# Performance work log

Measured on AMD Instinct MI355X. Metric: run time of the kernel, lower is better.

## Reference

```python
import jax, jax.numpy as jnp
import numpy as np

EMB = 1024
HEADS = 16
DH = EMB // HEADS


def setup_inputs() -> dict:
    key = jax.random.key(0)
    ks = jax.random.split(key, 9)
    B, S = 4, 2048
    scale = 1.0 / np.sqrt(EMB)
    x = jax.random.normal(ks[0], (B, S, EMB), dtype=jnp.float32)
    Wq = jax.random.normal(ks[1], (EMB, EMB), dtype=jnp.float32) * scale
    Wk = jax.random.normal(ks[2], (EMB, EMB), dtype=jnp.float32) * scale
    Wv = jax.random.normal(ks[3], (EMB, EMB), dtype=jnp.float32) * scale
    Wo = jax.random.normal(ks[4], (EMB, EMB), dtype=jnp.float32) * scale
    bq = jnp.zeros((EMB,), jnp.float32)
    bk = jnp.zeros((EMB,), jnp.float32)
    bv = jnp.zeros((EMB,), jnp.float32)
    bo = jnp.zeros((EMB,), jnp.float32)
    return {"x": x, "Wq": Wq, "bq": bq, "Wk": Wk, "bk": bk,
            "Wv": Wv, "bv": bv, "Wo": Wo, "bo": bo}


def _split_heads(t):
    B, S, _ = t.shape
    return t.reshape(B, S, HEADS, DH).transpose(0, 2, 1, 3)  # [B,H,S,Dh]


def reference(x, Wq, bq, Wk, bk, Wv, bv, Wo, bo):
    q = _split_heads(x @ Wq + bq)
    k = _split_heads(x @ Wk + bk)
    v = _split_heads(x @ Wv + bv)
    # scaled dot-product attention, full [B,H,S,S] score matrix as in source
    logits = jnp.einsum("bhqd,bhkd->bhqk", q, k) / jnp.sqrt(jnp.float32(DH))
    attn = jax.nn.softmax(logits, axis=-1)
    ctx = jnp.einsum("bhqk,bhkd->bhqd", attn, v)
    B, _, S, _ = ctx.shape
    concat = ctx.transpose(0, 2, 1, 3).reshape(B, S, EMB)
    return concat @ Wo + bo
```

## Files before the change

### kernel.cpp

```cpp
#include <hip/hip_runtime.h>
#include <hip/hip_bf16.h>
#include <stdint.h>

typedef __bf16 bf16;
typedef __bf16 bf16x4 __attribute__((ext_vector_type(4)));
typedef __bf16 bf16x8 __attribute__((ext_vector_type(8)));
typedef float f32x4 __attribute__((ext_vector_type(4)));

__device__ __forceinline__ void async_ld16(const void* g, void* l) {
  __builtin_amdgcn_global_load_lds(
      (__attribute__((address_space(1))) void*)(void*)(g),
      (__attribute__((address_space(3))) void*)(l), 16, 0, 0);
}

__device__ __forceinline__ bf16 fast_bf16(float f) {
  uint32_t u = (__float_as_uint(f) + 0x8000u) >> 16;
  union { uint16_t s; bf16 b; } cv;
  cv.s = (uint16_t)u;
  return cv.b;
}

__device__ __forceinline__ uint32_t pack_bf16(float lo, float hi) {
  return __builtin_amdgcn_perm(__float_as_uint(hi) + 0x8000u,
                               __float_as_uint(lo) + 0x8000u, 0x07060302u);
}

__global__ __launch_bounds__(256) void cast_f32_bf16(const float* __restrict__ in,
                                                     bf16* __restrict__ out, int n) {
  int i = (blockIdx.x * 256 + threadIdx.x) * 4;
  if (i < n) {
    float4 f = *(const float4*)(in + i);
    uint2 o;
    o.x = pack_bf16(f.x, f.y);
    o.y = pack_bf16(f.z, f.w);
    *(uint2*)(out + i) = o;
  }
}

__global__ __launch_bounds__(256) void transpose_weights(const float* __restrict__ Wq,
                                                         const float* __restrict__ Wk,
                                                         const float* __restrict__ Wv,
                                                         const float* __restrict__ Wo,
                                                         bf16* __restrict__ Wt,
                                                         bf16* __restrict__ Wot) {
  __shared__ bf16 tile[64][66];
  int z = blockIdx.z;
  const float* src = z == 0 ? Wq : (z == 1 ? Wk : (z == 2 ? Wv : Wo));
  bf16* dst = z == 0 ? Wt : (z == 1 ? Wt + 1048576 : (z == 2 ? Wt + 2097152 : Wot));
  int r0 = blockIdx.x * 64, c0 = blockIdx.y * 64;
  int t = threadIdx.x;
#pragma unroll
  for (int i = 0; i < 16; ++i) {
    int idx = t + i * 256;
    int r = idx >> 6, c = idx & 63;
    tile[r][c] = fast_bf16(src[(size_t)(r0 + r) * 1024 + (c0 + c)]);
  }
  __syncthreads();
#pragma unroll
  for (int i = 0; i < 16; ++i) {
    int idx = t + i * 256;
    int c = idx >> 6, r = idx & 63;
    dst[(size_t)(c0 + c) * 1024 + (r0 + r)] = tile[r][c];
  }
}

__device__ __forceinline__ void gemm128_mainloop(const bf16* __restrict__ A,
                                                 const bf16* __restrict__ Bt, int K,
                                                 int rowBase, int colBase,
                                                 bf16* As, bf16* Bs,
                                                 f32x4 (&acc)[4][4]) {
  int t = threadIdx.x, lane = t & 63, w = t >> 6;
  int wM = w >> 1, wN = w & 1, quad = lane >> 4, l15 = lane & 15;
  int r_off = lane >> 3;
  int c_sw = (((lane & 7) ^ r_off) << 3);
  int sw = l15 & 7;
  for (int k0 = 0; k0 < K; k0 += 64) {
    __syncthreads();
#pragma unroll
    for (int i = 0; i < 4; ++i) {
      int e = i * 2048 + w * 512;
      int row = (e >> 6) + r_off;
      async_ld16(A + (size_t)(rowBase + row) * K + (k0 + c_sw), As + e);
      async_ld16(Bt + (size_t)(colBase + row) * K + (k0 + c_sw), Bs + e);
    }
    __syncthreads();
#pragma unroll
    for (int ks = 0; ks < 2; ++ks) {
      int co = (((ks * 4 + quad) ^ sw) << 3);
      bf16x8 af[4], bfr[4];
#pragma unroll
      for (int mi = 0; mi < 4; ++mi)
        af[mi] = *(const bf16x8*)(As + (wM * 64 + mi * 16 + l15) * 64 + co);
#pragma unroll
      for (int ni = 0; ni < 4; ++ni)
        bfr[ni] = *(const bf16x8*)(Bs + (wN * 64 + ni * 16 + l15) * 64 + co);
#pragma unroll
      for (int mi = 0; mi < 4; ++mi)
#pragma unroll
        for (int ni = 0; ni < 4; ++ni)
          acc[mi][ni] = __builtin_amdgcn_mfma_f32_16x16x32_bf16(af[mi], bfr[ni], acc[mi][ni], 0, 0, 0);
    }
  }
}

__global__ __launch_bounds__(512, 2) void gemm_qkv(const bf16* __restrict__ X,
                                                   const bf16* __restrict__ Wt,
                                                   const float* __restrict__ bq,
                                                   const float* __restrict__ bk,
                                                   const float* __restrict__ bv,
                                                   bf16* __restrict__ Qo,
                                                   bf16* __restrict__ Ko,
                                                   bf16* __restrict__ Vto) {
  __shared__ alignas(16) bf16 smem[2][24576];

  int t = threadIdx.x, lane = t & 63, w = t >> 6;
  int wM = w >> 1, wN = w & 1, quad = lane >> 4, l15 = lane & 15;
  int r_off = lane >> 3;
  int c_sw = (((lane & 7) ^ r_off) << 3);
  int sw = l15 & 7;
  int rowBase = blockIdx.y * 256, colBase = blockIdx.x * 128;

  f32x4 acc[4][4];
  f32x4 z = {0.f, 0.f, 0.f, 0.f};
#pragma unroll
  for (int mi = 0; mi < 4; ++mi)
#pragma unroll
    for (int ni = 0; ni < 4; ++ni) acc[mi][ni] = z;

#pragma unroll
  for (int i = 0; i < 4; ++i) {
    int e = (w * 4 + i) * 512;
    int row = (e >> 6) + r_off;
    async_ld16(X + (size_t)(rowBase + row) * 1024 + c_sw, smem[0] + e);
  }
#pragma unroll
  for (int i = 0; i < 2; ++i) {
    int e = (w * 2 + i) * 512;
    int row = (e >> 6) + r_off;
    async_ld16(Wt + (size_t)(colBase + row) * 1024 + c_sw, smem[0] + 16384 + e);
  }
  __syncthreads();

  for (int kt = 0; kt < 16; ++kt) {
    int cur = kt & 1;
    const bf16* As = smem[cur];
    const bf16* Bs = smem[cur] + 16384;
    bf16* Asn = smem[cur ^ 1];
    bf16* Bsn = smem[cur ^ 1] + 16384;
    int kn = (kt + 1) * 64;

    bf16x8 af[4], bfr[2];

    if (kt < 15) {
#pragma unroll
      for (int i = 0; i < 4; ++i) {
        int e = (w * 4 + i) * 512;
        int row = (e >> 6) + r_off;
        async_ld16(X + (size_t)(rowBase + row) * 1024 + (kn + c_sw), Asn + e);
      }
    }
    {
      int co = ((quad ^ sw) << 3);
#pragma unroll
      for (int mi = 0; mi < 4; ++mi)
        af[mi] = *(const bf16x8*)(As + (wM * 64 + mi * 16 + l15) * 64 + co);
      bfr[0] = *(const bf16x8*)(Bs + (wN * 64 + l15) * 64 + co);
      bfr[1] = *(const bf16x8*)(Bs + (wN * 64 + 16 + l15) * 64 + co);
      asm volatile("s_waitcnt lgkmcnt(0)" ::: "memory");
      __builtin_amdgcn_sched_barrier(0);
      __builtin_amdgcn_s_setprio(1);
#pragma unroll
      for (int mi = 0; mi < 4; ++mi) {
        acc[mi][0] = __builtin_amdgcn_mfma_f32_16x16x32_bf16(af[mi], bfr[0], acc[mi][0], 0, 0, 0);
        acc[mi][1] = __builtin_amdgcn_mfma_f32_16x16x32_bf16(af[mi], bfr[1], acc[mi][1], 0, 0, 0);
      }
      __builtin_amdgcn_s_setprio(0);
    }

    if (kt < 15) {
#pragma unroll
      for (int i = 0; i < 2; ++i) {
        int e = (w * 2 + i) * 512;
        int row = (e >> 6) + r_off;
        async_ld16(Wt + (size_t)(colBase + row) * 1024 + (kn + c_sw), Bsn + e);
      }
    }
    {
      int co = ((quad ^ sw) << 3);
      bfr[0] = *(const bf16x8*)(Bs + (wN * 64 + 32 + l15) * 64 + co);
      bfr[1] = *(const bf16x8*)(Bs + (wN * 64 + 48 + l15) * 64 + co);
      asm volatile("s_waitcnt lgkmcnt(0)" ::: "memory");
      __builtin_amdgcn_sched_barrier(0);
      __builtin_amdgcn_s_setprio(1);
#pragma unroll
      for (int mi = 0; mi < 4; ++mi) {
        acc[mi][2] = __builtin_amdgcn_mfma_f32_16x16x32_bf16(af[mi], bfr[0], acc[mi][2], 0, 0, 0);
        acc[mi][3] = __builtin_amdgcn_mfma_f32_16x16x32_bf16(af[mi], bfr[1], acc[mi][3], 0, 0, 0);
      }
      __builtin_amdgcn_s_setprio(0);
    }

    {
      int co = (((4 + quad) ^ sw) << 3);
#pragma unroll
      for (int mi = 0; mi < 4; ++mi)
        af[mi] = *(const bf16x8*)(As + (wM * 64 + mi * 16 + l15) * 64 + co);
      bfr[0] = *(const bf16x8*)(Bs + (wN * 64 + l15) * 64 + co);
      bfr[1] = *(const bf16x8*)(Bs + (wN * 64 + 16 + l15) * 64 + co);
      asm volatile("s_waitcnt lgkmcnt(0)" ::: "memory");
      __builtin_amdgcn_sched_barrier(0);
      __builtin_amdgcn_s_setprio(1);
#pragma unroll
      for (int mi = 0; mi < 4; ++mi) {
        acc[mi][0] = __builtin_amdgcn_mfma_f32_16x16x32_bf16(af[mi], bfr[0], acc[mi][0], 0, 0, 0);
        acc[mi][1] = __builtin_amdgcn_mfma_f32_16x16x32_bf16(af[mi], bfr[1], acc[mi][1], 0, 0, 0);
      }
      __builtin_amdgcn_s_setprio(0);
    }

    {
      int co = (((4 + quad) ^ sw) << 3);
      bfr[0] = *(const bf16x8*)(Bs + (wN * 64 + 32 + l15) * 64 + co);
      bfr[1] = *(const bf16x8*)(Bs + (wN * 64 + 48 + l15) * 64 + co);
      asm volatile("s_waitcnt lgkmcnt(0)" ::: "memory");
      __builtin_amdgcn_sched_barrier(0);
      __builtin_amdgcn_s_setprio(1);
#pragma unroll
      for (int mi = 0; mi < 4; ++mi) {
        acc[mi][2] = __builtin_amdgcn_mfma_f32_16x16x32_bf16(af[mi], bfr[0], acc[mi][2], 0, 0, 0);
        acc[mi][3] = __builtin_amdgcn_mfma_f32_16x16x32_bf16(af[mi], bfr[1], acc[mi][3], 0, 0, 0);
      }
      __builtin_amdgcn_s_setprio(0);
    }

    __syncthreads();
  }

  int which = colBase >> 10;
  int baseh = (colBase & 1023) >> 6;
  int b = rowBase >> 11, s0 = rowBase & 2047;
  bf16* ep = smem[0];

  if (which == 2) {
#pragma unroll
    for (int hp = 0; hp < 2; ++hp) {
      __syncthreads();
      if (wN == hp) {
#pragma unroll
        for (int mi = 0; mi < 4; ++mi)
#pragma unroll
          for (int ni = 0; ni < 4; ++ni) {
            int d = ni * 16 + l15;
            float bb = bv[(colBase & 1023) + hp * 64 + d];
            int sl = wM * 64 + mi * 16 + quad * 4;
            uint2 pv;
            pv.x = pack_bf16(acc[mi][ni][0] + bb, acc[mi][ni][1] + bb);
            pv.y = pack_bf16(acc[mi][ni][2] + bb, acc[mi][ni][3] + bb);
            *(uint2*)(ep + d * 264 + sl) = pv;
          }
      }
      __syncthreads();
      int hg = baseh + hp;
#pragma unroll
      for (int it = 0; it < 4; ++it) {
        int idx = t + it * 512;
        int d = idx >> 5, c = idx & 31;
        bf16x8 vv = *(const bf16x8*)(ep + d * 264 + c * 8);
        *(bf16x8*)(Vto + (((size_t)((b << 4) + hg) << 6) + d) * 2048 + s0 + c * 8) = vv;
      }
    }
  } else {
    const float* bias = which == 0 ? bq : bk;
    bf16* dst = which == 0 ? Qo : Ko;
    float scale = which == 0 ? 0.125f * 1.44269504f : 1.0f;
#pragma unroll
    for (int hp = 0; hp < 2; ++hp) {
      __syncthreads();
      if (wN == hp) {
#pragma unroll
        for (int mi = 0; mi < 4; ++mi)
#pragma unroll
          for (int ni = 0; ni < 4; ++ni) {
            int d = ni * 16 + l15;
            float bb = bias[(colBase & 1023) + hp * 64 + d];
            int m = wM * 64 + mi * 16 + quad * 4;
#pragma unroll
            for (int r = 0; r < 4; ++r)
              ep[(m + r) * 72 + d] = fast_bf16((acc[mi][ni][r] + bb) * scale);
          }
      }
      __syncthreads();
      int hg = baseh + hp;
      bf16* gbase = dst + ((((size_t)((b << 4) + hg)) * 2048 + s0) << 6);
#pragma unroll
      for (int it = 0; it < 4; ++it) {
        int idx = t + it * 512;
        int m = idx >> 3, c = idx & 7;
        bf16x8 vv = *(const bf16x8*)(ep + m * 72 + c * 8);
        *(bf16x8*)(gbase + m * 64 + c * 8) = vv;
      }
    }
  }
}

__global__ __launch_bounds__(256) void gemm_out(const bf16* __restrict__ Cb,
                                                const bf16* __restrict__ Wot,
                                                const float* __restrict__ bo,
                                                float* __restrict__ out) {
  __shared__ alignas(16) bf16 As[128 * 64];
  __shared__ alignas(16) bf16 Bs[128 * 64];
  f32x4 acc[4][4];
  f32x4 z = {0.f, 0.f, 0.f, 0.f};
#pragma unroll
  for (int mi = 0; mi < 4; ++mi)
#pragma unroll
    for (int ni = 0; ni < 4; ++ni) acc[mi][ni] = z;
  int rowBase = blockIdx.y * 128, colBase = blockIdx.x * 128;
  gemm128_mainloop(Cb, Wot, 1024, rowBase, colBase, As, Bs, acc);

  int t = threadIdx.x, lane = t & 63, w = t >> 6;
  int wM = w >> 1, wN = w & 1, quad = lane >> 4, l15 = lane & 15;
#pragma unroll
  for (int mi = 0; mi < 4; ++mi)
#pragma unroll
    for (int ni = 0; ni < 4; ++ni) {
      int n = colBase + wN * 64 + ni * 16 + l15;
      float bb = bo[n];
#pragma unroll
      for (int r = 0; r < 4; ++r) {
        int m = rowBase + wM * 64 + mi * 16 + quad * 4 + r;
        out[(size_t)m * 1024 + n] = acc[mi][ni][r] + bb;
      }
    }
}

__global__ __launch_bounds__(256, 2) void attn(const bf16* __restrict__ Q,
                                               const bf16* __restrict__ Kg,
                                               const bf16* __restrict__ Vt,
                                               bf16* __restrict__ ctx) {
  __shared__ alignas(16) bf16 QPs[256 * 64];
  __shared__ alignas(16) bf16 Ks[2][4096];
  __shared__ alignas(16) bf16 Vs[2][4096];

  int t = threadIdx.x, lane = t & 63, w = t >> 6;
  int quad = lane >> 4, l15 = lane & 15;
  int r_off = lane >> 3;
  int c_sw = (((lane & 7) ^ r_off) << 3);
  int sw = l15 & 7;
  int bh = blockIdx.x;
  int q0 = blockIdx.y * 256;
  const bf16* Qp = Q + ((size_t)bh * 2048 + q0) * 64;
  const bf16* Kp = Kg + (size_t)bh * 2048 * 64;
  const bf16* Vp = Vt + (size_t)bh * 64 * 2048;

#pragma unroll
  for (int i = 0; i < 8; ++i) {
    int e = w * 4096 + i * 512;
    int row = (e >> 6) + r_off;
    async_ld16(Qp + (size_t)row * 64 + c_sw, QPs + e);
  }
#pragma unroll
  for (int i = 0; i < 2; ++i) {
    int e = w * 1024 + i * 512;
    int row = (e >> 6) + r_off;
    async_ld16(Kp + (size_t)row * 64 + c_sw, Ks[0] + e);
    async_ld16(Vp + (size_t)row * 2048 + c_sw, Vs[0] + e);
  }
  __syncthreads();

  bf16x8 qf[2][4];
#pragma unroll
  for (int ks = 0; ks < 2; ++ks)
#pragma unroll
    for (int qi = 0; qi < 4; ++qi)
      qf[ks][qi] = *(const bf16x8*)(QPs + (w * 64 + qi * 16 + l15) * 64 + (((ks * 4 + quad) ^ sw) << 3));
  asm volatile("s_waitcnt lgkmcnt(0)" ::: "memory");

  bf16* Ps = QPs + w * 4096;

  bf16 one1 = (bf16)1.0f;
  bf16x8 ones = {one1, one1, one1, one1, one1, one1, one1, one1};

  f32x4 o[4][4];
  f32x4 ol[4];
  f32x4 z = {0.f, 0.f, 0.f, 0.f};
#pragma unroll
  for (int mi = 0; mi < 4; ++mi) {
    ol[mi] = z;
#pragma unroll
    for (int ni = 0; ni < 4; ++ni) o[mi][ni] = z;
  }

  for (int kt = 0; kt < 32; ++kt) {
    int cur = kt & 1;
    if (kt < 31) {
      int kn = (kt + 1) * 64;
#pragma unroll
      for (int i = 0; i < 2; ++i) {
        int e = w * 1024 + i * 512;
        int row = (e >> 6) + r_off;
        async_ld16(Kp + (size_t)(kn + row) * 64 + c_sw, Ks[cur ^ 1] + e);
        async_ld16(Vp + (size_t)row * 2048 + kn + c_sw, Vs[cur ^ 1] + e);
      }
    }
    const bf16* Kc = Ks[cur];
    const bf16* Vc = Vs[cur];

    f32x4 sA[2][4];
#pragma unroll
    for (int ki = 0; ki < 2; ++ki)
#pragma unroll
      for (int qi = 0; qi < 4; ++qi) sA[ki][qi] = z;
    __builtin_amdgcn_s_setprio(1);
#pragma unroll
    for (int ks = 0; ks < 2; ++ks) {
      int co = (((ks * 4 + quad) ^ sw) << 3);
      bf16x8 kf0 = *(const bf16x8*)(Kc + (l15) * 64 + co);
      bf16x8 kf1 = *(const bf16x8*)(Kc + (16 + l15) * 64 + co);
#pragma unroll
      for (int qi = 0; qi < 4; ++qi) {
        sA[0][qi] = __builtin_amdgcn_mfma_f32_16x16x32_bf16(kf0, qf[ks][qi], sA[0][qi], 0, 0, 0);
        sA[1][qi] = __builtin_amdgcn_mfma_f32_16x16x32_bf16(kf1, qf[ks][qi], sA[1][qi], 0, 0, 0);
      }
    }
    __builtin_amdgcn_s_setprio(0);
#pragma unroll
    for (int qi = 0; qi < 4; ++qi)
#pragma unroll
      for (int ki = 0; ki < 2; ++ki) {
        float p0 = __builtin_amdgcn_exp2f(sA[ki][qi][0]);
        float p1 = __builtin_amdgcn_exp2f(sA[ki][qi][1]);
        float p2 = __builtin_amdgcn_exp2f(sA[ki][qi][2]);
        float p3 = __builtin_amdgcn_exp2f(sA[ki][qi][3]);
        uint2 pb;
        pb.x = pack_bf16(p0, p1);
        pb.y = pack_bf16(p2, p3);
        int cs = (ki * 2 + (quad >> 1)) ^ sw;
        *(uint2*)(Ps + (qi * 16 + l15) * 64 + cs * 8 + (quad & 1) * 4) = pb;
      }

    f32x4 sB[2][4];
#pragma unroll
    for (int ki = 0; ki < 2; ++ki)
#pragma unroll
      for (int qi = 0; qi < 4; ++qi) sB[ki][qi] = z;
    __builtin_amdgcn_s_setprio(1);
#pragma unroll
    for (int ks = 0; ks < 2; ++ks) {
      int co = (((ks * 4 + quad) ^ sw) << 3);
      bf16x8 kf2 = *(const bf16x8*)(Kc + (32 + l15) * 64 + co);
      bf16x8 kf3 = *(const bf16x8*)(Kc + (48 + l15) * 64 + co);
#pragma unroll
      for (int qi = 0; qi < 4; ++qi) {
        sB[0][qi] = __builtin_amdgcn_mfma_f32_16x16x32_bf16(kf2, qf[ks][qi], sB[0][qi], 0, 0, 0);
        sB[1][qi] = __builtin_amdgcn_mfma_f32_16x16x32_bf16(kf3, qf[ks][qi], sB[1][qi], 0, 0, 0);
      }
    }
    __builtin_amdgcn_s_setprio(0);

    asm volatile("s_waitcnt lgkmcnt(0)" ::: "memory");

    {
      int co = ((quad ^ sw) << 3);
      bf16x8 pf[4], vf[4];
#pragma unroll
      for (int mi = 0; mi < 4; ++mi)
        pf[mi] = *(const bf16x8*)(Ps + (mi * 16 + l15) * 64 + co);
#pragma unroll
      for (int ni = 0; ni < 4; ++ni)
        vf[ni] = *(const bf16x8*)(Vc + (ni * 16 + l15) * 64 + co);
      __builtin_amdgcn_s_setprio(1);
#pragma unroll
      for (int mi = 0; mi < 4; ++mi) {
#pragma unroll
        for (int ni = 0; ni < 4; ++ni)
          o[mi][ni] = __builtin_amdgcn_mfma_f32_16x16x32_bf16(pf[mi], vf[ni], o[mi][ni], 0, 0, 0);
        ol[mi] = __builtin_amdgcn_mfma_f32_16x16x32_bf16(pf[mi], ones, ol[mi], 0, 0, 0);
      }
      __builtin_amdgcn_s_setprio(0);
    }

#pragma unroll
    for (int qi = 0; qi < 4; ++qi)
#pragma unroll
      for (int ki = 0; ki < 2; ++ki) {
        float p0 = __builtin_amdgcn_exp2f(sB[ki][qi][0]);
        float p1 = __builtin_amdgcn_exp2f(sB[ki][qi][1]);
        float p2 = __builtin_amdgcn_exp2f(sB[ki][qi][2]);
        float p3 = __builtin_amdgcn_exp2f(sB[ki][qi][3]);
        uint2 pb;
        pb.x = pack_bf16(p0, p1);
        pb.y = pack_bf16(p2, p3);
        int cs = (ki * 2 + 4 + (quad >> 1)) ^ sw;
        *(uint2*)(Ps + (qi * 16 + l15) * 64 + cs * 8 + (quad & 1) * 4) = pb;
      }

    asm volatile("s_waitcnt lgkmcnt(0)" ::: "memory");

    {
      int co = (((4 + quad) ^ sw) << 3);
      bf16x8 pf[4], vf[4];
#pragma unroll
      for (int mi = 0; mi < 4; ++mi)
        pf[mi] = *(const bf16x8*)(Ps + (mi * 16 + l15) * 64 + co);
#pragma unroll
      for (int ni = 0; ni < 4; ++ni)
        vf[ni] = *(const bf16x8*)(Vc + (ni * 16 + l15) * 64 + co);
      __builtin_amdgcn_s_setprio(1);
#pragma unroll
      for (int mi = 0; mi < 4; ++mi) {
#pragma unroll
        for (int ni = 0; ni < 4; ++ni)
          o[mi][ni] = __builtin_amdgcn_mfma_f32_16x16x32_bf16(pf[mi], vf[ni], o[mi][ni], 0, 0, 0);
        ol[mi] = __builtin_amdgcn_mfma_f32_16x16x32_bf16(pf[mi], ones, ol[mi], 0, 0, 0);
      }
      __builtin_amdgcn_s_setprio(0);
    }

    __syncthreads();
  }

  int b = bh >> 4, h = bh & 15;
#pragma unroll
  for (int mi = 0; mi < 4; ++mi) {
    float rl[4];
#pragma unroll
    for (int r = 0; r < 4; ++r) rl[r] = 1.0f / ol[mi][r];
#pragma unroll
    for (int ni = 0; ni < 4; ++ni) {
      int col = h * 64 + ni * 16 + l15;
#pragma unroll
      for (int r = 0; r < 4; ++r) {
        int q = q0 + w * 64 + mi * 16 + quad * 4 + r;
        ctx[(size_t)(b * 2048 + q) * 1024 + col] = fast_bf16(o[mi][ni][r] * rl[r]);
      }
    }
  }
}

extern "C" void kernel_launch(void* const* d_in, const int* in_sizes, int n_in,
                              void* d_out, int out_size, void* d_ws, size_t ws_size,
                              hipStream_t stream) {
  const float* x  = (const float*)d_in[0];
  const float* Wq = (const float*)d_in[1];
  const float* bq = (const float*)d_in[2];
  const float* Wk = (const float*)d_in[3];
  const float* bk = (const float*)d_in[4];
  const float* Wv = (const float*)d_in[5];
  const float* bv = (const float*)d_in[6];
  const float* Wo = (const float*)d_in[7];
  const float* bo = (const float*)d_in[8];
  float* out = (float*)d_out;

  char* ws = (char*)d_ws;
  const size_t MB = 1048576;
  bf16* xb  = (bf16*)(ws);
  bf16* Wt  = (bf16*)(ws + 16 * MB);
  bf16* Wot = (bf16*)(ws + 22 * MB);
  bf16* Qb  = (bf16*)(ws + 24 * MB);
  bf16* Kb  = (bf16*)(ws + 40 * MB);
  bf16* Vtb = (bf16*)(ws + 56 * MB);
  bf16* Cx  = (bf16*)(ws + 72 * MB);

  cast_f32_bf16<<<8192, 256, 0, stream>>>(x, xb, 8388608);
  transpose_weights<<<dim3(16, 16, 4), 256, 0, stream>>>(Wq, Wk, Wv, Wo, Wt, Wot);
  gemm_qkv<<<dim3(24, 32, 1), 512, 0, stream>>>(xb, Wt, bq, bk, bv, Qb, Kb, Vtb);
  attn<<<dim3(64, 8, 1), 256, 0, stream>>>(Qb, Kb, Vtb, Cx);
  gemm_out<<<dim3(8, 64, 1), 256, 0, stream>>>(Cx, Wot, bo, out);
}
```

Before: 263.6 us.

## Share pipelined 256x128 GEMM mainloop with out-proj; register-prefetch K/V in attention

Moves the software-pipelined, double-buffered 256x128 GEMM mainloop into a shared helper, and switches the output projection to it with 512-thread blocks and 256-row tiles. This replaces the older single-buffered 128x128 loop, which synchronised twice per k-step. In attention, the double-buffered LDS async K/V loads become global-to-register prefetches into a single LDS buffer, stored after an extra barrier. The smaller LDS footprint allows a launch-bounds hint of 3 blocks per CU, trading load/compute overlap and an additional sync for higher occupancy.

```diff
diff --git a/kernel.cpp b/kernel.cpp
--- a/kernel.cpp
+++ b/kernel.cpp
@@ -64,42 +64,123 @@
   }
 }
 
-__device__ __forceinline__ void gemm128_mainloop(const bf16* __restrict__ A,
-                                                 const bf16* __restrict__ Bt, int K,
+__device__ __forceinline__ void gemm256_mainloop(const bf16* __restrict__ A,
+                                                 const bf16* __restrict__ Bt,
                                                  int rowBase, int colBase,
-                                                 bf16* As, bf16* Bs,
-                                                 f32x4 (&acc)[4][4]) {
+                                                 bf16* smem, f32x4 (&acc)[4][4]) {
   int t = threadIdx.x, lane = t & 63, w = t >> 6;
   int wM = w >> 1, wN = w & 1, quad = lane >> 4, l15 = lane & 15;
   int r_off = lane >> 3;
   int c_sw = (((lane & 7) ^ r_off) << 3);
   int sw = l15 & 7;
-  for (int k0 = 0; k0 < K; k0 += 64) {
-    __syncthreads();
-#pragma unroll
-    for (int i = 0; i < 4; ++i) {
-      int e = i * 2048 + w * 512;
-      int row = (e >> 6) + r_off;
-      async_ld16(A + (size_t)(rowBase + row) * K + (k0 + c_sw), As + e);
-      async_ld16(Bt + (size_t)(colBase + row) * K + (k0 + c_sw), Bs + e);
-    }
-    __syncthreads();
-#pragma unroll
-    for (int ks = 0; ks < 2; ++ks) {
-      int co = (((ks * 4 + quad) ^ sw) << 3);
-      bf16x8 af[4], bfr[4];
+
+#pragma unroll
+  for (int i = 0; i < 4; ++i) {
+    int e = (w * 4 + i) * 512;
+    int row = (e >> 6) + r_off;
+    async_ld16(A + (size_t)(rowBase + row) * 1024 + c_sw, smem + e);
+  }
+#pragma unroll
+  for (int i = 0; i < 2; ++i) {
+    int e = (w * 2 + i) * 512;
+    int row = (e >> 6) + r_off;
+    async_ld16(Bt + (size_t)(colBase + row) * 1024 + c_sw, smem + 16384 + e);
+  }
+  __syncthreads();
+
+  for (int kt = 0; kt < 16; ++kt) {
+    int cur = kt & 1;
+    const bf16* As = smem + cur * 24576;
+    const bf16* Bs = As + 16384;
+    bf16* Asn = smem + (cur ^ 1) * 24576;
+    bf16* Bsn = Asn + 16384;
+    int kn = (kt + 1) * 64;
+
+    bf16x8 af[4], bfr[2];
+
+    if (kt < 15) {
+#pragma unroll
+      for (int i = 0; i < 4; ++i) {
+        int e = (w * 4 + i) * 512;
+        int row = (e >> 6) + r_off;
+        async_ld16(A + (size_t)(rowBase + row) * 1024 + (kn + c_sw), Asn + e);
+      }
+    }
+    {
+      int co = ((quad ^ sw) << 3);
 #pragma unroll
       for (int mi = 0; mi < 4; ++mi)
         af[mi] = *(const bf16x8*)(As + (wM * 64 + mi * 16 + l15) * 64 + co);
-#pragma unroll
-      for (int ni = 0; ni < 4; ++ni)
-        bfr[ni] = *(const bf16x8*)(Bs + (wN * 64 + ni * 16 + l15) * 64 + co);
+      bfr[0] = *(const bf16x8*)(Bs + (wN * 64 + l15) * 64 + co);
+      bfr[1] = *(const bf16x8*)(Bs + (wN * 64 + 16 + l15) * 64 + co);
+      asm volatile("s_waitcnt lgkmcnt(0)" ::: "memory");
+      __builtin_amdgcn_sched_barrier(0);
+      __builtin_amdgcn_s_setprio(1);
+#pragma unroll
+      for (int mi = 0; mi < 4; ++mi) {
+        acc[mi][0] = __builtin_amdgcn_mfma_f32_16x16x32_bf16(af[mi], bfr[0], acc[mi][0], 0, 0, 0);
+        acc[mi][1] = __builtin_amdgcn_mfma_f32_16x16x32_bf16(af[mi], bfr[1], acc[mi][1], 0, 0, 0);
+      }
+      __builtin_amdgcn_s_setprio(0);
+    }
+
+    if (kt < 15) {
+#pragma unroll
+      for (int i = 0; i < 2; ++i) {
+        int e = (w * 2 + i) * 512;
+        int row = (e >> 6) + r_off;
+        async_ld16(Bt + (size_t)(colBase + row) * 1024 + (kn + c_sw), Bsn + e);
+      }
+    }
+    {
+      int co = ((quad ^ sw) << 3);
+      bfr[0] = *(const bf16x8*)(Bs + (wN * 64 + 32 + l15) * 64 + co);
+      bfr[1] = *(const bf16x8*)(Bs + (wN * 64 + 48 + l15) * 64 + co);
+      asm volatile("s_waitcnt lgkmcnt(0)" ::: "memory");
+      __builtin_amdgcn_sched_barrier(0);
+      __builtin_amdgcn_s_setprio(1);
+#pragma unroll
+      for (int mi = 0; mi < 4; ++mi) {
+        acc[mi][2] = __builtin_amdgcn_mfma_f32_16x16x32_bf16(af[mi], bfr[0], acc[mi][2], 0, 0, 0);
+        acc[mi][3] = __builtin_amdgcn_mfma_f32_16x16x32_bf16(af[mi], bfr[1], acc[mi][3], 0, 0, 0);
+      }
+      __builtin_amdgcn_s_setprio(0);
+    }
+
+    {
+      int co = (((4 + quad) ^ sw) << 3);
 #pragma unroll
       for (int mi = 0; mi < 4; ++mi)
-#pragma unroll
-        for (int ni = 0; ni < 4; ++ni)
-          acc[mi][ni] = __builtin_amdgcn_mfma_f32_16x16x32_bf16(af[mi], bfr[ni], acc[mi][ni], 0, 0, 0);
-    }
+        af[mi] = *(const bf16x8*)(As + (wM * 64 + mi * 16 + l15) * 64 + co);
+      bfr[0] = *(const bf16x8*)(Bs + (wN * 64 + l15) * 64 + co);
+      bfr[1] = *(const bf16x8*)(Bs + (wN * 64 + 16 + l15) * 64 + co);
+      asm volatile("s_waitcnt lgkmcnt(0)" ::: "memory");
+      __builtin_amdgcn_sched_barrier(0);
+      __builtin_amdgcn_s_setprio(1);
+#pragma unroll
+      for (int mi = 0; mi < 4; ++mi) {
+        acc[mi][0] = __builtin_amdgcn_mfma_f32_16x16x32_bf16(af[mi], bfr[0], acc[mi][0], 0, 0, 0);
+        acc[mi][1] = __builtin_amdgcn_mfma_f32_16x16x32_bf16(af[mi], bfr[1], acc[mi][1], 0, 0, 0);
+      }
+      __builtin_amdgcn_s_setprio(0);
+    }
+
+    {
+      int co = (((4 + quad) ^ sw) << 3);
+      bfr[0] = *(const bf16x8*)(Bs + (wN * 64 + 32 + l15) * 64 + co);
+      bfr[1] = *(const bf16x8*)(Bs + (wN * 64 + 48 + l15) * 64 + co);
+      asm volatile("s_waitcnt lgkmcnt(0)" ::: "memory");
+      __builtin_amdgcn_sched_barrier(0);
+      __builtin_amdgcn_s_setprio(1);
+#pragma unroll
+      for (int mi = 0; mi < 4; ++mi) {
+        acc[mi][2] = __builtin_amdgcn_mfma_f32_16x16x32_bf16(af[mi], bfr[0], acc[mi][2], 0, 0, 0);
+        acc[mi][3] = __builtin_amdgcn_mfma_f32_16x16x32_bf16(af[mi], bfr[1], acc[mi][3], 0, 0, 0);
+      }
+      __builtin_amdgcn_s_setprio(0);
+    }
+
+    __syncthreads();
   }
 }
 
@@ -111,13 +192,10 @@
                                                    bf16* __restrict__ Qo,
                                                    bf16* __restrict__ Ko,
                                                    bf16* __restrict__ Vto) {
-  __shared__ alignas(16) bf16 smem[2][24576];
+  __shared__ alignas(16) bf16 smem[2 * 24576];
 
   int t = threadIdx.x, lane = t & 63, w = t >> 6;
   int wM = w >> 1, wN = w & 1, quad = lane >> 4, l15 = lane & 15;
-  int r_off = lane >> 3;
-  int c_sw = (((lane & 7) ^ r_off) << 3);
-  int sw = l15 & 7;
   int rowBase = blockIdx.y * 256, colBase = blockIdx.x * 128;
 
   f32x4 acc[4][4];
@@ -127,119 +205,12 @@
 #pragma unroll
     for (int ni = 0; ni < 4; ++ni) acc[mi][ni] = z;
 
-#pragma unroll
-  for (int i = 0; i < 4; ++i) {
-    int e = (w * 4 + i) * 512;
-    int row = (e >> 6) + r_off;
-    async_ld16(X + (size_t)(rowBase + row) * 1024 + c_sw, smem[0] + e);
-  }
-#pragma unroll
-  for (int i = 0; i < 2; ++i) {
-    int e = (w * 2 + i) * 512;
-    int row = (e >> 6) + r_off;
-    async_ld16(Wt + (size_t)(colBase + row) * 1024 + c_sw, smem[0] + 16384 + e);
-  }
-  __syncthreads();
-
-  for (int kt = 0; kt < 16; ++kt) {
-    int cur = kt & 1;
-    const bf16* As = smem[cur];
-    const bf16* Bs = smem[cur] + 16384;
-    bf16* Asn = smem[cur ^ 1];
-    bf16* Bsn = smem[cur ^ 1] + 16384;
-    int kn = (kt + 1) * 64;
-
-    bf16x8 af[4], bfr[2];
-
-    if (kt < 15) {
-#pragma unroll
-      for (int i = 0; i < 4; ++i) {
-        int e = (w * 4 + i) * 512;
-        int row = (e >> 6) + r_off;
-        async_ld16(X + (size_t)(rowBase + row) * 1024 + (kn + c_sw), Asn + e);
-      }
-    }
-    {
-      int co = ((quad ^ sw) << 3);
-#pragma unroll
-      for (int mi = 0; mi < 4; ++mi)
-        af[mi] = *(const bf16x8*)(As + (wM * 64 + mi * 16 + l15) * 64 + co);
-      bfr[0] = *(const bf16x8*)(Bs + (wN * 64 + l15) * 64 + co);
-      bfr[1] = *(const bf16x8*)(Bs + (wN * 64 + 16 + l15) * 64 + co);
-      asm volatile("s_waitcnt lgkmcnt(0)" ::: "memory");
-      __builtin_amdgcn_sched_barrier(0);
-      __builtin_amdgcn_s_setprio(1);
-#pragma unroll
-      for (int mi = 0; mi < 4; ++mi) {
-        acc[mi][0] = __builtin_amdgcn_mfma_f32_16x16x32_bf16(af[mi], bfr[0], acc[mi][0], 0, 0, 0);
-        acc[mi][1] = __builtin_amdgcn_mfma_f32_16x16x32_bf16(af[mi], bfr[1], acc[mi][1], 0, 0, 0);
-      }
-      __builtin_amdgcn_s_setprio(0);
-    }
-
-    if (kt < 15) {
-#pragma unroll
-      for (int i = 0; i < 2; ++i) {
-        int e = (w * 2 + i) * 512;
-        int row = (e >> 6) + r_off;
-        async_ld16(Wt + (size_t)(colBase + row) * 1024 + (kn + c_sw), Bsn + e);
-      }
-    }
-    {
-      int co = ((quad ^ sw) << 3);
-      bfr[0] = *(const bf16x8*)(Bs + (wN * 64 + 32 + l15) * 64 + co);
-      bfr[1] = *(const bf16x8*)(Bs + (wN * 64 + 48 + l15) * 64 + co);
-      asm volatile("s_waitcnt lgkmcnt(0)" ::: "memory");
-      __builtin_amdgcn_sched_barrier(0);
-      __builtin_amdgcn_s_setprio(1);
-#pragma unroll
-      for (int mi = 0; mi < 4; ++mi) {
-        acc[mi][2] = __builtin_amdgcn_mfma_f32_16x16x32_bf16(af[mi], bfr[0], acc[mi][2], 0, 0, 0);
-        acc[mi][3] = __builtin_amdgcn_mfma_f32_16x16x32_bf16(af[mi], bfr[1], acc[mi][3], 0, 0, 0);
-      }
-      __builtin_amdgcn_s_setprio(0);
-    }
-
-    {
-      int co = (((4 + quad) ^ sw) << 3);
-#pragma unroll
-      for (int mi = 0; mi < 4; ++mi)
-        af[mi] = *(const bf16x8*)(As + (wM * 64 + mi * 16 + l15) * 64 + co);
-      bfr[0] = *(const bf16x8*)(Bs + (wN * 64 + l15) * 64 + co);
-      bfr[1] = *(const bf16x8*)(Bs + (wN * 64 + 16 + l15) * 64 + co);
-      asm volatile("s_waitcnt lgkmcnt(0)" ::: "memory");
-      __builtin_amdgcn_sched_barrier(0);
-      __builtin_amdgcn_s_setprio(1);
-#pragma unroll
-      for (int mi = 0; mi < 4; ++mi) {
-        acc[mi][0] = __builtin_amdgcn_mfma_f32_16x16x32_bf16(af[mi], bfr[0], acc[mi][0], 0, 0, 0);
-        acc[mi][1] = __builtin_amdgcn_mfma_f32_16x16x32_bf16(af[mi], bfr[1], acc[mi][1], 0, 0, 0);
-      }
-      __builtin_amdgcn_s_setprio(0);
-    }
-
-    {
-      int co = (((4 + quad) ^ sw) << 3);
-      bfr[0] = *(const bf16x8*)(Bs + (wN * 64 + 32 + l15) * 64 + co);
-      bfr[1] = *(const bf16x8*)(Bs + (wN * 64 + 48 + l15) * 64 + co);
-      asm volatile("s_waitcnt lgkmcnt(0)" ::: "memory");
-      __builtin_amdgcn_sched_barrier(0);
-      __builtin_amdgcn_s_setprio(1);
-#pragma unroll
-      for (int mi = 0; mi < 4; ++mi) {
-        acc[mi][2] = __builtin_amdgcn_mfma_f32_16x16x32_bf16(af[mi], bfr[0], acc[mi][2], 0, 0, 0);
-        acc[mi][3] = __builtin_amdgcn_mfma_f32_16x16x32_bf16(af[mi], bfr[1], acc[mi][3], 0, 0, 0);
-      }
-      __builtin_amdgcn_s_setprio(0);
-    }
-
-    __syncthreads();
-  }
+  gemm256_mainloop(X, Wt, rowBase, colBase, smem, acc);
 
   int which = colBase >> 10;
   int baseh = (colBase & 1023) >> 6;
   int b = rowBase >> 11, s0 = rowBase & 2047;
-  bf16* ep = smem[0];
+  bf16* ep = smem;
 
   if (which == 2) {
 #pragma unroll
@@ -303,23 +274,25 @@
   }
 }
 
-__global__ __launch_bounds__(256) void gemm_out(const bf16* __restrict__ Cb,
-                                                const bf16* __restrict__ Wot,
-                                                const float* __restrict__ bo,
-                                                float* __restrict__ out) {
-  __shared__ alignas(16) bf16 As[128 * 64];
-  __shared__ alignas(16) bf16 Bs[128 * 64];
+__global__ __launch_bounds__(512, 2) void gemm_out(const bf16* __restrict__ Cb,
+                                                   const bf16* __restrict__ Wot,
+                                                   const float* __restrict__ bo,
+                                                   float* __restrict__ out) {
+  __shared__ alignas(16) bf16 smem[2 * 24576];
+
+  int t = threadIdx.x, lane = t & 63, w = t >> 6;
+  int wM = w >> 1, wN = w & 1, quad = lane >> 4, l15 = lane & 15;
+  int rowBase = blockIdx.y * 256, colBase = blockIdx.x * 128;
+
   f32x4 acc[4][4];
   f32x4 z = {0.f, 0.f, 0.f, 0.f};
 #pragma unroll
   for (int mi = 0; mi < 4; ++mi)
 #pragma unroll
     for (int ni = 0; ni < 4; ++ni) acc[mi][ni] = z;
-  int rowBase = blockIdx.y * 128, colBase = blockIdx.x * 128;
-  gemm128_mainloop(Cb, Wot, 1024, rowBase, colBase, As, Bs, acc);
-
-  int t = threadIdx.x, lane = t & 63, w = t >> 6;
-  int wM = w >> 1, wN = w & 1, quad = lane >> 4, l15 = lane & 15;
+
+  gemm256_mainloop(Cb, Wot, rowBase, colBase, smem, acc);
+
 #pragma unroll
   for (int mi = 0; mi < 4; ++mi)
 #pragma unroll
@@ -334,13 +307,13 @@
     }
 }
 
-__global__ __launch_bounds__(256, 2) void attn(const bf16* __restrict__ Q,
+__global__ __launch_bounds__(256, 3) void attn(const bf16* __restrict__ Q,
                                                const bf16* __restrict__ Kg,
                                                const bf16* __restrict__ Vt,
                                                bf16* __restrict__ ctx) {
   __shared__ alignas(16) bf16 QPs[256 * 64];
-  __shared__ alignas(16) bf16 Ks[2][4096];
-  __shared__ alignas(16) bf16 Vs[2][4096];
+  __shared__ alignas(16) bf16 Ks[4096];
+  __shared__ alignas(16) bf16 Vs[4096];
 
   int t = threadIdx.x, lane = t & 63, w = t >> 6;
   int quad = lane >> 4, l15 = lane & 15;
@@ -363,8 +336,8 @@
   for (int i = 0; i < 2; ++i) {
     int e = w * 1024 + i * 512;
     int row = (e >> 6) + r_off;
-    async_ld16(Kp + (size_t)row * 64 + c_sw, Ks[0] + e);
-    async_ld16(Vp + (size_t)row * 2048 + c_sw, Vs[0] + e);
+    async_ld16(Kp + (size_t)row * 64 + c_sw, Ks + e);
+    async_ld16(Vp + (size_t)row * 2048 + c_sw, Vs + e);
   }
   __syncthreads();
 
@@ -392,19 +365,19 @@
   }
 
   for (int kt = 0; kt < 32; ++kt) {
-    int cur = kt & 1;
+    bf16x8 kpre[2], vpre[2];
     if (kt < 31) {
       int kn = (kt + 1) * 64;
 #pragma unroll
       for (int i = 0; i < 2; ++i) {
         int e = w * 1024 + i * 512;
         int row = (e >> 6) + r_off;
-        async_ld16(Kp + (size_t)(kn + row) * 64 + c_sw, Ks[cur ^ 1] + e);
-        async_ld16(Vp + (size_t)row * 2048 + kn + c_sw, Vs[cur ^ 1] + e);
-      }
-    }
-    const bf16* Kc = Ks[cur];
-    const bf16* Vc = Vs[cur];
+        kpre[i] = *(const bf16x8*)(Kp + (size_t)(kn + row) * 64 + c_sw);
+        vpre[i] = *(const bf16x8*)(Vp + (size_t)row * 2048 + kn + c_sw);
+      }
+    }
+    const bf16* Kc = Ks;
+    const bf16* Vc = Vs;
 
     f32x4 sA[2][4];
 #pragma unroll
@@ -517,6 +490,15 @@
       __builtin_amdgcn_s_setprio(0);
     }
 
+    __syncthreads();
+    if (kt < 31) {
+#pragma unroll
+      for (int i = 0; i < 2; ++i) {
+        int e = w * 1024 + i * 512;
+        *(bf16x8*)(Ks + e + lane * 8) = kpre[i];
+        *(bf16x8*)(Vs + e + lane * 8) = vpre[i];
+      }
+    }
     __syncthreads();
   }
 
@@ -566,5 +548,5 @@
   transpose_weights<<<dim3(16, 16, 4), 256, 0, stream>>>(Wq, Wk, Wv, Wo, Wt, Wot);
   gemm_qkv<<<dim3(24, 32, 1), 512, 0, stream>>>(xb, Wt, bq, bk, bv, Qb, Kb, Vtb);
   attn<<<dim3(64, 8, 1), 256, 0, stream>>>(Qb, Kb, Vtb, Cx);
-  gemm_out<<<dim3(8, 64, 1), 256, 0, stream>>>(Cx, Wot, bo, out);
-}
+  gemm_out<<<dim3(8, 32, 1), 512, 0, stream>>>(Cx, Wot, bo, out);
+}
```

Measured after the change: 445.3 us. 69.0% more time.
